# Kernel optimization log

Hardware: AMD Instinct MI355X
Metric: run time of the kernel (lower is better)

The kernel has to match this reference:

```python
import jax, jax.numpy as jnp
import numpy as np

H = 4          # attention_heads
TOPK = 101     # hard-coded [:101] in ContextModule.forward
EPS = 1e-5     # nn.LayerNorm default eps


def _linear(x, w, b):
    # torch nn.Linear: y = x @ W^T + b
    return x @ w.T + b


def _layer_norm(x, g, b):
    mu = jnp.mean(x, axis=-1, keepdims=True)
    var = jnp.var(x, axis=-1, keepdims=True)
    return (x - mu) * jax.lax.rsqrt(var + EPS) * g + b


def setup_inputs() -> dict:
    key = jax.random.key(0)
    ks = jax.random.split(key, 12)
    D, N, B, T = 512, 2000, 8, 1024
    s = 0.02
    f32 = jnp.float32
    return {
        "context_emb": jax.random.normal(ks[0], (N, D), f32),
        "encoder_out": jax.random.normal(ks[1], (B, T, D), f32),
        "wq": jax.random.normal(ks[2], (D, D), f32) * s,
        "bq": jnp.zeros((D,), f32),
        "wk": jax.random.normal(ks[3], (D, D), f32) * s,
        "bk": jnp.zeros((D,), f32),
        "wv": jax.random.normal(ks[4], (D, D), f32) * s,
        "bv": jnp.zeros((D,), f32),
        "wo": jax.random.normal(ks[5], (D, D), f32) * s,
        "bo": jnp.zeros((D,), f32),
        "w_comb": jax.random.normal(ks[6], (D, D), f32) * s,
        "b_comb": jnp.zeros((D,), f32),
        "ln_g": jnp.ones((D,), f32),
        "ln_b": jnp.zeros((D,), f32),
    }


def reference(context_emb, encoder_out, wq, bq, wk, bk, wv, bv, wo, bo,
              w_comb, b_comb, ln_g, ln_b):
    biasing_score = 1.0
    B, T, D = encoder_out.shape
    dk = D // H
    scale = 1.0 / np.sqrt(dk).astype(np.float32)

    # expand context to batch: [B, N, D]
    ctx = jnp.broadcast_to(context_emb, (B,) + context_emb.shape)

    # --- pass 1: attention matrix for scoring (get_attn_mat) ---
    q = _linear(encoder_out, wq, bq).reshape(B, T, H, dk).transpose(0, 2, 1, 3)  # bhtd
    k = _linear(ctx, wk, bk).reshape(B, -1, H, dk).transpose(0, 2, 1, 3)         # bhnd
    scores = jnp.einsum('bhtd,bhnd->bhtn', q, k) * scale
    attn = jax.nn.softmax(scores, axis=-1)                                        # [B,H,T,N]

    # attn_mat[0].sum(0).sum(0): per-context-phrase aggregate score -> [N]
    context_scores = attn[0].sum(axis=(0, 1))
    # torch.sort(descending)[1][:101] == top-101 indices by score
    _, idx = jax.lax.top_k(context_scores, TOPK)

    # gather filtered context embeddings: [B, 101, D]
    ctx_f = ctx[:, idx, :]

    # --- pass 2: full MHA on filtered context ---
    k2 = _linear(ctx_f, wk, bk).reshape(B, TOPK, H, dk).transpose(0, 2, 1, 3)
    v2 = _linear(ctx_f, wv, bv).reshape(B, TOPK, H, dk).transpose(0, 2, 1, 3)
    a2 = jax.nn.softmax(jnp.einsum('bhtd,bhnd->bhtn', q, k2) * scale, axis=-1)
    o = jnp.einsum('bhtn,bhnd->bhtd', a2, v2).transpose(0, 2, 1, 3).reshape(B, T, D)
    o = _linear(o, wo, bo)

    # combiner + residual + LayerNorm
    out = encoder_out + _linear(o, w_comb, b_comb) * biasing_score
    return _layer_norm(out, ln_g, ln_b)
```

## Files before the change

kernel.cpp:

```cpp
#include <hip/hip_runtime.h>
#include <hip/hip_bf16.h>


typedef short bhalf8 __attribute__((ext_vector_type(8)));
typedef float f32x4 __attribute__((ext_vector_type(4)));

#define SCALE 0.08838834764831845f

#define OFF_QBF    ((size_t)0)
#define OFF_RB     ((size_t)6193152)
#define OFF_TMP    ((size_t)8290304)
#define OFF_PART   (OFF_TMP)
#define OFF_CS     (OFF_TMP + 1024000)
#define OFF_IDX    (OFF_TMP + 1026048)
#define OFF_RSP    (OFF_TMP + 1026176)
#define OFF_CEBF   ((size_t)12484608)
#define OFF_K2BF   ((size_t)13022608)
#define OFF_V2TP   ((size_t)13074608)
#define OFF_WQBF   ((size_t)13107376)
#define OFF_WKBF   ((size_t)13238448)
#define OFF_WVBF   ((size_t)13369520)
#define OFF_WCBF   ((size_t)13500592)
#define OFF_WOTBF  ((size_t)13631664)
#define OFF_WC2BF  ((size_t)13762736)
#define OFF_BC2    ((size_t)13893808)

__device__ __forceinline__ float bf2f(short u) {
    union { float f; unsigned int i; } x;
    x.i = ((unsigned int)(unsigned short)u) << 16;
    return x.f;
}
__device__ __forceinline__ ushort f2b(float f) {
    union { float f; unsigned int i; } x; x.f = f;
    return (ushort)((x.i + 0x7fff + ((x.i >> 16) & 1)) >> 16);
}

__device__ __forceinline__ void gld16(ushort* lds, const ushort* g) {
    __builtin_amdgcn_global_load_lds(
        (const __attribute__((address_space(1))) unsigned int*)g,
        (__attribute__((address_space(3))) unsigned int*)lds, 16, 0, 0);
}

__global__ __launch_bounds__(256) void prep_kernel(
    const float* __restrict__ enc, const float* __restrict__ ce,
    const float* __restrict__ wq, const float* __restrict__ wk,
    const float* __restrict__ wv, const float* __restrict__ wc,
    const float* __restrict__ wo, const float* __restrict__ bo,
    const float* __restrict__ bcb,
    ushort* __restrict__ encbf, ushort* __restrict__ cebf,
    ushort* __restrict__ wqbf, ushort* __restrict__ wkbf,
    ushort* __restrict__ wvbf, ushort* __restrict__ wcbf,
    ushort* __restrict__ v2tp, ushort* __restrict__ wotbf,
    float* __restrict__ bc2)
{
    __shared__ float tile[32][33];
    const int b = blockIdx.x, tid = threadIdx.x;
    const float* s; ushort* d; int n4, base;
    if (b < 4096)      { s = enc; d = encbf; n4 = 1048576; base = b; }
    else if (b < 5096) { s = ce;  d = cebf;  n4 = 256000;  base = b - 4096; }
    else if (b < 5352) { s = wq;  d = wqbf;  n4 = 65536;   base = b - 5096; }
    else if (b < 5608) { s = wk;  d = wkbf;  n4 = 65536;   base = b - 5352; }
    else if (b < 5864) { s = wv;  d = wvbf;  n4 = 65536;   base = b - 5608; }
    else if (b < 6120) { s = wc;  d = wcbf;  n4 = 65536;   base = b - 5864; }
    else if (b < 6152) {
        const int i = (b - 6120) * 256 + tid;
        ((uint4*)v2tp)[i] = make_uint4(0u, 0u, 0u, 0u);
        return;
    } else if (b < 6154) {
        const int dd = (b - 6152) * 256 + tid;
        float acc = bcb[dd];
        const float4* wr = (const float4*)(wc + (size_t)dd * 512);
        const float4* br = (const float4*)bo;
        for (int m4 = 0; m4 < 128; ++m4) {
            const float4 w4 = wr[m4], b4 = br[m4];
            acc += w4.x * b4.x + w4.y * b4.y + w4.z * b4.z + w4.w * b4.w;
        }
        bc2[dd] = acc;
        return;
    } else {
        const int b2 = b - 6154;
        const int bx = (b2 & 15) * 32, by = (b2 >> 4) * 32;
        const int tx = tid & 31, ty = tid >> 5;
        #pragma unroll
        for (int rr = 0; rr < 4; ++rr)
            tile[ty + 8 * rr][tx] = wo[(size_t)(by + ty + 8 * rr) * 512 + bx + tx];
        __syncthreads();
        #pragma unroll
        for (int rr = 0; rr < 4; ++rr)
            wotbf[(size_t)(bx + ty + 8 * rr) * 512 + by + tx] =
                f2b(tile[tx][ty + 8 * rr]);
        return;
    }
    const int i = base * 256 + tid;
    if (i >= n4) return;
    const float4 v = ((const float4*)s)[i];
    ushort4 r;
    r.x = f2b(v.x); r.y = f2b(v.y); r.z = f2b(v.z); r.w = f2b(v.w);
    ((ushort4*)d)[i] = r;
}

__device__ __forceinline__ void stage_ab(
    const ushort* gA, const ushort* gB0, const ushort* gB1, int k0,
    ushort* As, ushort* Bs, int wave)
{
    gld16(As + wave * 512,        gA  + k0);
    gld16(As + 2048 + wave * 512, gA  + k0 + 32);
    gld16(Bs + wave * 512,        gB0 + k0);
    gld16(Bs + 4096 + wave * 512, gB0 + k0 + 32);
    gld16(Bs + 2048 + wave * 512, gB1 + k0);
    gld16(Bs + 6144 + wave * 512, gB1 + k0 + 32);
}

__device__ __forceinline__ void gemm_body_512(
    const ushort* A, const ushort* W, const float* bias, ushort* Cbf,
    int M, int bm, int bn, ushort* As, ushort* Bs, int rowA)
{
    const int tid = threadIdx.x;
    const int wave = tid >> 6, lane = tid & 63;
    const int wm = wave >> 1, wn = wave & 1;
    const int mr = lane & 15, g = lane >> 4;

    f32x4 acc[2][4];
    #pragma unroll
    for (int i = 0; i < 2; ++i)
        #pragma unroll
        for (int j = 0; j < 4; ++j)
            #pragma unroll
            for (int p = 0; p < 4; ++p) acc[i][j][p] = 0.f;

    const int r0 = tid >> 2, c0 = tid & 3;
    const int cA = (c0 ^ (r0 & 3)) * 8;
    const ushort* gA  = A + (size_t)rowA * 512 + cA;
    const ushort* gB0 = W + (size_t)(bn + r0) * 512 + cA;
    const ushort* gB1 = W + (size_t)(bn + r0 + 64) * 512 + cA;

    stage_ab(gA, gB0, gB1, 0, As, Bs, wave);
    for (int k0 = 0; k0 < 512; k0 += 64) {
        const int cur = (k0 >> 6) & 1;
        ushort* Ac = As + cur * 4096;
        ushort* Bc = Bs + cur * 8192;
        __syncthreads();
        if (k0 + 64 < 512)
            stage_ab(gA, gB0, gB1, k0 + 64,
                     As + (cur ^ 1) * 4096, Bs + (cur ^ 1) * 8192, wave);
        const int ksw = (g ^ (mr & 3)) << 3;
        #pragma unroll
        for (int h = 0; h < 2; ++h) {
            bhalf8 a[2], b[4];
            #pragma unroll
            for (int i = 0; i < 2; ++i)
                a[i] = *(const bhalf8*)
                    &Ac[h * 2048 + (wm * 32 + i * 16 + mr) * 32 + ksw];
            #pragma unroll
            for (int j = 0; j < 4; ++j)
                b[j] = *(const bhalf8*)
                    &Bc[h * 4096 + (wn * 64 + j * 16 + mr) * 32 + ksw];
            #pragma unroll
            for (int i = 0; i < 2; ++i)
                #pragma unroll
                for (int j = 0; j < 4; ++j)
                    acc[i][j] = __builtin_amdgcn_mfma_f32_16x16x32_bf16(
                        a[i], b[j], acc[i][j], 0, 0, 0);
        }
    }

    #pragma unroll
    for (int i = 0; i < 2; ++i) {
        #pragma unroll
        for (int j = 0; j < 4; ++j) {
            const int gn = bn + wn * 64 + j * 16 + mr;
            const float bb = bias ? bias[gn] : 0.f;
            #pragma unroll
            for (int p = 0; p < 4; ++p) {
                const int gm = bm + wm * 32 + i * 16 + g * 4 + p;
                if (gm >= M) continue;
                Cbf[(size_t)gm * 512 + gn] = f2b(acc[i][j][p] + bb);
            }
        }
    }
}

__global__ __launch_bounds__(256) void qkc_gemm(
    const ushort* __restrict__ encbf, const ushort* __restrict__ cebf,
    const ushort* __restrict__ wcbf,
    const ushort* __restrict__ wqbf, const ushort* __restrict__ wkbf,
    const ushort* __restrict__ wotbf,
    const float* __restrict__ bq, const float* __restrict__ bk,
    ushort* __restrict__ qbf, ushort* __restrict__ kcbf,
    ushort* __restrict__ wc2bf)
{
    __shared__ __align__(16) ushort As[2 * 64 * 64];
    __shared__ __align__(16) ushort Bs[2 * 128 * 64];
    const int z = blockIdx.z;
    if (z == 1 && blockIdx.y >= 32) return;
    if (z == 2 && blockIdx.y >= 8) return;
    const ushort* A = (z == 0) ? encbf : (z == 1) ? cebf : wcbf;
    const ushort* W = (z == 0) ? wqbf : (z == 1) ? wkbf : wotbf;
    const float* bias = (z == 0) ? bq : (z == 1) ? bk : nullptr;
    ushort* C = (z == 0) ? qbf : (z == 1) ? kcbf : wc2bf;
    const int M = (z == 0) ? 8192 : (z == 1) ? 2000 : 512;
    const int bm = blockIdx.y * 64;
    const int rowA = min(bm + (threadIdx.x >> 2), M - 1);
    gemm_body_512(A, W, bias, C, M, bm, blockIdx.x * 128, As, Bs, rowA);
}

__device__ __forceinline__ void stage_ktile(
    ushort* Ks, const ushort* kcbf, int nt, int h, int w, int lane)
{
    #pragma unroll
    for (int it = 0; it < 8; ++it) {
        const int u = it * 256 + (w << 6) + lane;
        const int nl = u >> 4, c = u & 15;
        gld16(Ks + (size_t)(it * 256 + (w << 6)) * 8,
              kcbf + (size_t)(nt * 128 + nl) * 512 + (h << 7)
                   + ((c ^ (nl & 7)) << 3));
    }
}

__device__ __forceinline__ void score_tile(
    const ushort* Ks, const bhalf8* aq, int mr, int g, f32x4* sacc)
{
    #pragma unroll
    for (int jn = 0; jn < 8; ++jn)
        #pragma unroll
        for (int p = 0; p < 4; ++p) sacc[jn][p] = 0.f;
    #pragma unroll
    for (int kd = 0; kd < 4; ++kd) {
        #pragma unroll
        for (int jn = 0; jn < 8; ++jn) {
            const int n = (jn << 4) + mr;
            const bhalf8 bk = *(const bhalf8*)
                &Ks[(n << 7) + ((((kd << 2) + g) ^ (n & 7)) << 3)];
            sacc[jn] = __builtin_amdgcn_mfma_f32_16x16x32_bf16(
                aq[kd], bk, sacc[jn], 0, 0, 0);
        }
    }
}

__global__ __launch_bounds__(256) void rowsum_part(
    const ushort* __restrict__ qb, const ushort* __restrict__ kcbf,
    float* __restrict__ rsp)
{
    __shared__ __align__(16) ushort Ks[2 * 128 * 128];
    const int tid = threadIdx.x, w = tid >> 6, lane = tid & 63;
    const int mr = lane & 15, g = lane >> 4;
    const int h = blockIdx.y, nc = blockIdx.z;
    const int bm = blockIdx.x * 64;

    const ushort* qrow = qb + (size_t)(bm + (w << 4) + mr) * 512 + (h << 7);
    bhalf8 aq[4];
    #pragma unroll
    for (int kd = 0; kd < 4; ++kd)
        aq[kd] = *(const bhalf8*)(qrow + (g << 3) + (kd << 5));

    const int nt0 = nc * 2, nt1 = nc * 2 + 1;
    stage_ktile(Ks, kcbf, nt0, h, w, lane);
    __syncthreads();
    stage_ktile(Ks + 16384, kcbf, nt1, h, w, lane);

    float rsl[4] = {0.f, 0.f, 0.f, 0.f};
    f32x4 sacc[8];
    score_tile(Ks, aq, mr, g, sacc);
    #pragma unroll
    for (int jn = 0; jn < 8; ++jn) {
        const bool valid = nt0 * 128 + (jn << 4) + mr < 2000;
        #pragma unroll
        for (int p = 0; p < 4; ++p)
            rsl[p] += valid ? __expf(sacc[jn][p] * SCALE) : 0.f;
    }
    __syncthreads();
    score_tile(Ks + 16384, aq, mr, g, sacc);
    #pragma unroll
    for (int jn = 0; jn < 8; ++jn) {
        const bool valid = nt1 * 128 + (jn << 4) + mr < 2000;
        #pragma unroll
        for (int p = 0; p < 4; ++p)
            rsl[p] += valid ? __expf(sacc[jn][p] * SCALE) : 0.f;
    }

    #pragma unroll
    for (int off = 1; off <= 8; off <<= 1)
        #pragma unroll
        for (int p = 0; p < 4; ++p)
            rsl[p] += __shfl_xor(rsl[p], off);
    if (mr == 0) {
        #pragma unroll
        for (int p = 0; p < 4; ++p) {
            const int row = (h << 10) + bm + (w << 4) + (g << 2) + p;
            rsp[(size_t)row * 8 + nc] = rsl[p];
        }
    }
}

__global__ __launch_bounds__(256) void colsum_part(
    const ushort* __restrict__ qb, const ushort* __restrict__ kcbf,
    const float* __restrict__ rsp, float* __restrict__ part)
{
    __shared__ __align__(16) ushort Ks[2 * 128 * 128];
    const int tid = threadIdx.x, w = tid >> 6, lane = tid & 63;
    const int mr = lane & 15, g = lane >> 4;
    const int h = blockIdx.y, nc = blockIdx.z;
    const int bm = blockIdx.x * 64;
    const int slot = ((h * 16 + blockIdx.x) << 2) + w;

    const ushort* qrow = qb + (size_t)(bm + (w << 4) + mr) * 512 + (h << 7);
    bhalf8 aq[4];
    #pragma unroll
    for (int kd = 0; kd < 4; ++kd)
        aq[kd] = *(const bhalf8*)(qrow + (g << 3) + (kd << 5));

    float inv[4];
    #pragma unroll
    for (int p = 0; p < 4; ++p) {
        const int row = (h << 10) + bm + (w << 4) + (g << 2) + p;
        const float4 ra = *(const float4*)(rsp + (size_t)row * 8);
        const float4 rb = *(const float4*)(rsp + (size_t)row * 8 + 4);
        inv[p] = 1.f / (ra.x + ra.y + ra.z + ra.w + rb.x + rb.y + rb.z + rb.w);
    }

    const int nt0 = nc * 2, nt1 = nc * 2 + 1;
    stage_ktile(Ks, kcbf, nt0, h, w, lane);
    __syncthreads();
    stage_ktile(Ks + 16384, kcbf, nt1, h, w, lane);

    f32x4 sacc[8];
    #pragma unroll
    for (int t = 0; t < 2; ++t) {
        if (t == 1) __syncthreads();
        const int nt = t ? nt1 : nt0;
        score_tile(t ? Ks + 16384 : Ks, aq, mr, g, sacc);
        #pragma unroll
        for (int jn = 0; jn < 8; ++jn) {
            const int n = nt * 128 + (jn << 4) + mr;
            const bool valid = n < 2000;
            float cv = 0.f;
            #pragma unroll
            for (int p = 0; p < 4; ++p)
                cv += valid ? __expf(sacc[jn][p] * SCALE) * inv[p] : 0.f;
            cv += __shfl_xor(cv, 16);
            cv += __shfl_xor(cv, 32);
            if (g == 0 && valid) part[(size_t)slot * 2000 + n] = cv;
        }
    }
}

__global__ __launch_bounds__(256) void reduce_full_kernel(
    const float* __restrict__ part, float* __restrict__ cs)
{
    const int n = blockIdx.x * 256 + threadIdx.x;
    if (n >= 2000) return;
    float s = 0.f;
    for (int sl = 0; sl < 256; ++sl) s += part[(size_t)sl * 2000 + n];
    cs[n] = s;
}

__global__ void topk_kernel(const float* __restrict__ cs,
                            int* __restrict__ idx)
{
    const int lane = threadIdx.x;
    const unsigned long long below = (1ull << lane) - 1ull;

    unsigned key[32];
    #pragma unroll
    for (int i = 0; i < 32; ++i) {
        const int n = lane + 64 * i;
        const float s = (n < 2000) ? cs[n] : -1e30f;
        const unsigned u = __float_as_uint(s);
        key[i] = u ^ ((unsigned)((int)u >> 31) | 0x80000000u);
    }

    unsigned prefix = 0;
    int remaining = 101;
    for (int b = 31; b >= 0; --b) {
        const unsigned tgt = (prefix << 1) | 1u;
        int cnt = 0;
        #pragma unroll
        for (int i = 0; i < 32; ++i)
            cnt += (int)__popcll(__ballot((key[i] >> b) == tgt));
        if (cnt >= remaining) prefix = tgt;
        else { remaining -= cnt; prefix = prefix << 1; }
    }
    const unsigned T = prefix;

    int base = 0;
    #pragma unroll
    for (int i = 0; i < 32; ++i) {
        const unsigned long long m = __ballot(key[i] > T);
        if (key[i] > T) idx[base + (int)__popcll(m & below)] = lane + 64 * i;
        base += (int)__popcll(m);
    }
    int r = remaining;
    #pragma unroll
    for (int i = 0; i < 32; ++i) {
        const unsigned long long m = __ballot(key[i] == T);
        const int cb = (int)__popcll(m & below);
        if (key[i] == T && cb < r) idx[base + cb] = lane + 64 * i;
        const int take = min(r, (int)__popcll(m));
        base += take; r -= take;
    }
}

__global__ __launch_bounds__(256) void kv2_proj(
    const ushort* __restrict__ cebf, const int* __restrict__ idxbuf,
    const ushort* __restrict__ wkbf, const ushort* __restrict__ wvbf,
    const float* __restrict__ bk, const float* __restrict__ bv,
    ushort* __restrict__ k2bf, ushort* __restrict__ v2tp)
{
    __shared__ __align__(16) ushort As[2 * 64 * 64];
    __shared__ __align__(16) ushort Bs[2 * 128 * 64];
    const int z = blockIdx.z;
    const ushort* W = z ? wvbf : wkbf;
    const float* bias = z ? bv : bk;
    const int tid = threadIdx.x;
    const int wave = tid >> 6, lane = tid & 63;
    const int wm = wave >> 1, wn = wave & 1;
    const int mr = lane & 15, g = lane >> 4;
    const int bm = blockIdx.y * 64, bn = blockIdx.x * 128;

    f32x4 acc[2][4];
    #pragma unroll
    for (int i = 0; i < 2; ++i)
        #pragma unroll
        for (int j = 0; j < 4; ++j)
            #pragma unroll
            for (int p = 0; p < 4; ++p) acc[i][j][p] = 0.f;

    const int r0 = tid >> 2, c0 = tid & 3;
    const int cA = (c0 ^ (r0 & 3)) * 8;
    const int rA  = min(bm + r0, 100);
    const int srcrow = idxbuf[rA];
    const ushort* gA  = cebf + (size_t)srcrow * 512 + cA;
    const ushort* gB0 = W + (size_t)(bn + r0) * 512 + cA;
    const ushort* gB1 = W + (size_t)(bn + r0 + 64) * 512 + cA;

    stage_ab(gA, gB0, gB1, 0, As, Bs, wave);
    for (int k0 = 0; k0 < 512; k0 += 64) {
        const int cur = (k0 >> 6) & 1;
        ushort* Ac = As + cur * 4096;
        ushort* Bc = Bs + cur * 8192;
        __syncthreads();
        if (k0 + 64 < 512)
            stage_ab(gA, gB0, gB1, k0 + 64,
                     As + (cur ^ 1) * 4096, Bs + (cur ^ 1) * 8192, wave);
        const int ksw = (g ^ (mr & 3)) << 3;
        #pragma unroll
        for (int h = 0; h < 2; ++h) {
            bhalf8 a[2], b[4];
            #pragma unroll
            for (int i = 0; i < 2; ++i)
                a[i] = *(const bhalf8*)
                    &Ac[h * 2048 + (wm * 32 + i * 16 + mr) * 32 + ksw];
            #pragma unroll
            for (int j = 0; j < 4; ++j)
                b[j] = *(const bhalf8*)
                    &Bc[h * 4096 + (wn * 64 + j * 16 + mr) * 32 + ksw];
            #pragma unroll
            for (int i = 0; i < 2; ++i)
                #pragma unroll
                for (int j = 0; j < 4; ++j)
                    acc[i][j] = __builtin_amdgcn_mfma_f32_16x16x32_bf16(
                        a[i], b[j], acc[i][j], 0, 0, 0);
        }
    }

    #pragma unroll
    for (int i = 0; i < 2; ++i) {
        #pragma unroll
        for (int j = 0; j < 4; ++j) {
            const int gn = bn + wn * 64 + j * 16 + mr;
            const float bb = bias[gn];
            #pragma unroll
            for (int p = 0; p < 4; ++p) {
                const int gm = bm + wm * 32 + i * 16 + g * 4 + p;
                if (gm >= 101) continue;
                const ushort v = f2b(acc[i][j][p] + bb);
                if (z == 0) k2bf[(size_t)gm * 512 + gn] = v;
                else        v2tp[(size_t)gn * 128 + gm] = v;
            }
        }
    }
}

__global__ __launch_bounds__(512) void attn2_fused(
    const ushort* __restrict__ qb, const ushort* __restrict__ k2bf,
    const ushort* __restrict__ v2tp, ushort* __restrict__ obf)
{
    __shared__ __align__(16) ushort K2s[128 * 128];
    __shared__ __align__(16) ushort V2s[128 * 128];
    __shared__ __align__(16) ushort Ps[8 * 16 * 128];
    const int tid = threadIdx.x, w = tid >> 6, lane = tid & 63;
    const int mr = lane & 15, g = lane >> 4;
    const int h = blockIdx.y;
    const int bm = blockIdx.x * 128;

    #pragma unroll
    for (int it = 0; it < 4; ++it) {
        const int cl = tid + 512 * it;
        const int n = cl >> 4, c = cl & 15;
        uint4 kv = make_uint4(0u, 0u, 0u, 0u);
        if (n < 101)
            kv = *(const uint4*)(k2bf + (size_t)n * 512 + h * 128 + c * 8);
        *(uint4*)&K2s[(n << 7) + ((c ^ (n & 7)) << 3)] = kv;
        const uint4 vv = *(const uint4*)(v2tp + (((size_t)h << 7) + n) * 128 + c * 8);
        *(uint4*)&V2s[(n << 7) + ((c ^ (n & 7)) << 3)] = vv;
    }
    __syncthreads();

    f32x4 sacc[8];
    #pragma unroll
    for (int jn = 0; jn < 8; ++jn)
        #pragma unroll
        for (int p = 0; p < 4; ++p) sacc[jn][p] = 0.f;
    const ushort* qrow = qb + (size_t)(bm + (w << 4) + mr) * 512 + (h << 7);
    #pragma unroll
    for (int kd = 0; kd < 4; ++kd) {
        const bhalf8 aq = *(const bhalf8*)(qrow + (g << 3) + (kd << 5));
        #pragma unroll
        for (int jn = 0; jn < 8; ++jn) {
            const int n = (jn << 4) + mr;
            const bhalf8 bk = *(const bhalf8*)
                &K2s[(n << 7) + ((((kd << 2) + g) ^ (n & 7)) << 3)];
            sacc[jn] = __builtin_amdgcn_mfma_f32_16x16x32_bf16(aq, bk, sacc[jn], 0, 0, 0);
        }
    }

    float mrow[4] = {-1e30f, -1e30f, -1e30f, -1e30f};
    #pragma unroll
    for (int jn = 0; jn < 8; ++jn) {
        const bool valid = (jn < 6) || (jn == 6 && mr < 5);
        #pragma unroll
        for (int p = 0; p < 4; ++p) {
            const float s = valid ? sacc[jn][p] * SCALE : -1e30f;
            sacc[jn][p] = s;
            mrow[p] = fmaxf(mrow[p], s);
        }
    }
    #pragma unroll
    for (int off = 1; off <= 8; off <<= 1)
        #pragma unroll
        for (int p = 0; p < 4; ++p)
            mrow[p] = fmaxf(mrow[p], __shfl_xor(mrow[p], off));
    float srow[4] = {0.f, 0.f, 0.f, 0.f};
    #pragma unroll
    for (int jn = 0; jn < 8; ++jn)
        #pragma unroll
        for (int p = 0; p < 4; ++p) {
            const float e = __expf(sacc[jn][p] - mrow[p]);
            sacc[jn][p] = e;
            srow[p] += e;
        }
    #pragma unroll
    for (int off = 1; off <= 8; off <<= 1)
        #pragma unroll
        for (int p = 0; p < 4; ++p)
            srow[p] += __shfl_xor(srow[p], off);
    float inv[4];
    #pragma unroll
    for (int p = 0; p < 4; ++p) inv[p] = 1.f / srow[p];

    ushort* pw = Ps + (w << 11);
    #pragma unroll
    for (int jn = 0; jn < 8; ++jn) {
        const int cb = (jn << 1) + (mr >> 3);
        #pragma unroll
        for (int p = 0; p < 4; ++p) {
            const int r = (g << 2) + p;
            pw[(r << 7) + ((cb ^ (r & 7)) << 3) + (mr & 7)] =
                f2b(sacc[jn][p] * inv[p]);
        }
    }

    f32x4 oacc[8];
    #pragma unroll
    for (int jd = 0; jd < 8; ++jd)
        #pragma unroll
        for (int p = 0; p < 4; ++p) oacc[jd][p] = 0.f;
    #pragma unroll
    for (int kn = 0; kn < 4; ++kn) {
        const int ck = (kn << 2) + g;
        const bhalf8 ap = *(const bhalf8*)
            &pw[(mr << 7) + ((ck ^ (mr & 7)) << 3)];
        #pragma unroll
        for (int jd = 0; jd < 8; ++jd) {
            const int d = (jd << 4) + mr;
            const bhalf8 bv = *(const bhalf8*)
                &V2s[(d << 7) + ((ck ^ (d & 7)) << 3)];
            oacc[jd] = __builtin_amdgcn_mfma_f32_16x16x32_bf16(ap, bv, oacc[jd], 0, 0, 0);
        }
    }

    #pragma unroll
    for (int jd = 0; jd < 8; ++jd)
        #pragma unroll
        for (int p = 0; p < 4; ++p) {
            const int row = bm + (w << 4) + (g << 2) + p;
            obf[(size_t)row * 512 + (h << 7) + (jd << 4) + mr] = f2b(oacc[jd][p]);
        }
}

__device__ __forceinline__ void pl_stage(
    const ushort* gA, const ushort* gB, int k0,
    ushort* Asb, ushort* Bsb, int w)
{
    if (w < 2) {
        gld16(Asb + w * 512,        gA + k0);
        gld16(Asb + 1024 + w * 512, gA + k0 + 32);
    }
    #pragma unroll
    for (int r = 0; r < 8; ++r) {
        const int nb = r * 4 + w;
        gld16(Bsb + nb * 512,         gB + nb * 8192 + k0);
        gld16(Bsb + 16384 + nb * 512, gB + nb * 8192 + k0 + 32);
    }
}

__global__ __launch_bounds__(256) void proj_ln(
    const ushort* __restrict__ obf, const ushort* __restrict__ wc2bf,
    const float* __restrict__ bc2, const float* __restrict__ enc,
    const float* __restrict__ gw, const float* __restrict__ bta,
    float* __restrict__ out)
{
    __shared__ __align__(16) ushort As[2 * 2048];
    __shared__ __align__(16) ushort Bs[2 * 32768];
    __shared__ float red1[2][32], red2[2][32];
    const int tid = threadIdx.x, w = tid >> 6, lane = tid & 63;
    const int mr = lane & 15, gq = lane >> 4;
    const int rh = w & 1, ch = w >> 1;
    const int bm = blockIdx.x * 32;

    f32x4 acc[16];
    #pragma unroll
    for (int j = 0; j < 16; ++j)
        #pragma unroll
        for (int p = 0; p < 4; ++p) acc[j][p] = 0.f;

    const int lr = lane >> 2, lc = lane & 3;
    const int swc = (lc ^ (lr & 3)) * 8;
    const ushort* gA = obf + (size_t)(bm + ((w & 1) << 4) + lr) * 512 + swc;
    const ushort* gB = wc2bf + (size_t)lr * 512 + swc;

    pl_stage(gA, gB, 0, As, Bs, w);
    for (int k0 = 0; k0 < 512; k0 += 64) {
        const int cur = (k0 >> 6) & 1;
        ushort* Ac = As + cur * 2048;
        ushort* Bc = Bs + cur * 32768;
        __syncthreads();
        if (k0 + 64 < 512)
            pl_stage(gA, gB, k0 + 64,
                     As + (cur ^ 1) * 2048, Bs + (cur ^ 1) * 32768, w);
        const int ksw = (gq ^ (mr & 3)) << 3;
        #pragma unroll
        for (int h = 0; h < 2; ++h) {
            const bhalf8 a = *(const bhalf8*)
                &Ac[h * 1024 + (((rh << 4) + mr) << 5) + ksw];
            #pragma unroll
            for (int j = 0; j < 16; ++j) {
                const int n = (ch << 8) + (j << 4) + mr;
                const bhalf8 b = *(const bhalf8*)
                    &Bc[h * 16384 + (n << 5) + ksw];
                acc[j] = __builtin_amdgcn_mfma_f32_16x16x32_bf16(a, b, acc[j], 0, 0, 0);
            }
        }
    }

    float s1[4] = {0.f, 0.f, 0.f, 0.f}, s2[4] = {0.f, 0.f, 0.f, 0.f};
    #pragma unroll
    for (int j = 0; j < 16; ++j) {
        const int gcol = (ch << 8) + (j << 4) + mr;
        const float bb = bc2[gcol];
        #pragma unroll
        for (int p = 0; p < 4; ++p) {
            const int grow = bm + (rh << 4) + (gq << 2) + p;
            const float x = acc[j][p] + bb + enc[(size_t)grow * 512 + gcol];
            acc[j][p] = x;
            s1[p] += x;
            s2[p] += x * x;
        }
    }
    #pragma unroll
    for (int off = 1; off <= 8; off <<= 1)
        #pragma unroll
        for (int p = 0; p < 4; ++p) {
            s1[p] += __shfl_xor(s1[p], off);
            s2[p] += __shfl_xor(s2[p], off);
        }
    if (mr == 0) {
        #pragma unroll
        for (int p = 0; p < 4; ++p) {
            red1[ch][(rh << 4) + (gq << 2) + p] = s1[p];
            red2[ch][(rh << 4) + (gq << 2) + p] = s2[p];
        }
    }
    __syncthreads();
    float mu[4], rstd[4];
    #pragma unroll
    for (int p = 0; p < 4; ++p) {
        const int ri = (rh << 4) + (gq << 2) + p;
        const float t1 = red1[0][ri] + red1[1][ri];
        const float t2 = red2[0][ri] + red2[1][ri];
        const float m = t1 * (1.f / 512.f);
        mu[p] = m;
        rstd[p] = rsqrtf(t2 * (1.f / 512.f) - m * m + 1e-5f);
    }
    #pragma unroll
    for (int j = 0; j < 16; ++j) {
        const int gcol = (ch << 8) + (j << 4) + mr;
        const float gg = gw[gcol], bb = bta[gcol];
        #pragma unroll
        for (int p = 0; p < 4; ++p) {
            const int grow = bm + (rh << 4) + (gq << 2) + p;
            out[(size_t)grow * 512 + gcol] = (acc[j][p] - mu[p]) * rstd[p] * gg + bb;
        }
    }
}

extern "C" void kernel_launch(void* const* d_in, const int* in_sizes, int n_in,
                              void* d_out, int out_size, void* d_ws, size_t ws_size,
                              hipStream_t stream)
{
    const float* ce  = (const float*)d_in[0];
    const float* enc = (const float*)d_in[1];
    const float* wq  = (const float*)d_in[2];
    const float* bq  = (const float*)d_in[3];
    const float* wk  = (const float*)d_in[4];
    const float* bk  = (const float*)d_in[5];
    const float* wv  = (const float*)d_in[6];
    const float* bv  = (const float*)d_in[7];
    const float* wo  = (const float*)d_in[8];
    const float* bo  = (const float*)d_in[9];
    const float* wc  = (const float*)d_in[10];
    const float* bcb = (const float*)d_in[11];
    const float* lng = (const float*)d_in[12];
    const float* lnb = (const float*)d_in[13];
    float* ws  = (float*)d_ws;
    float* out = (float*)d_out;

    ushort* qbf    = (ushort*)(ws + OFF_QBF);
    ushort* encbf  = (ushort*)(ws + OFF_RB);
    ushort* kcbf   = (ushort*)(ws + OFF_RB);
    ushort* obf    = (ushort*)(ws + OFF_RB);
    float*  part   = ws + OFF_PART;
    float*  cs     = ws + OFF_CS;
    int*    idx    = (int*)(ws + OFF_IDX);
    float*  rsp    = ws + OFF_RSP;
    ushort* cebf   = (ushort*)(ws + OFF_CEBF);
    ushort* k2bf   = (ushort*)(ws + OFF_K2BF);
    ushort* v2tp   = (ushort*)(ws + OFF_V2TP);
    ushort* wqbf   = (ushort*)(ws + OFF_WQBF);
    ushort* wkbf   = (ushort*)(ws + OFF_WKBF);
    ushort* wvbf   = (ushort*)(ws + OFF_WVBF);
    ushort* wcbf   = (ushort*)(ws + OFF_WCBF);
    ushort* wotbf  = (ushort*)(ws + OFF_WOTBF);
    ushort* wc2bf  = (ushort*)(ws + OFF_WC2BF);
    float*  bc2    = ws + OFF_BC2;

    prep_kernel<<<6410, 256, 0, stream>>>(enc, ce, wq, wk, wv, wc, wo, bo, bcb,
                                          encbf, cebf, wqbf, wkbf, wvbf, wcbf,
                                          v2tp, wotbf, bc2);
    qkc_gemm<<<dim3(4, 128, 3), 256, 0, stream>>>(encbf, cebf, wcbf,
                                                  wqbf, wkbf, wotbf,
                                                  bq, bk, qbf, kcbf, wc2bf);
    rowsum_part<<<dim3(16, 4, 8), 256, 0, stream>>>(qbf, kcbf, rsp);
    colsum_part<<<dim3(16, 4, 8), 256, 0, stream>>>(qbf, kcbf, rsp, part);
    reduce_full_kernel<<<8, 256, 0, stream>>>(part, cs);
    topk_kernel<<<1, 64, 0, stream>>>(cs, idx);
    kv2_proj<<<dim3(4, 2, 2), 256, 0, stream>>>(cebf, idx, wkbf, wvbf, bk, bv,
                                                k2bf, v2tp);
    attn2_fused<<<dim3(64, 4), 512, 0, stream>>>(qbf, k2bf, v2tp, obf);
    proj_ln<<<256, 256, 0, stream>>>(obf, wc2bf, bc2, enc, lng, lnb, out);
    (void)in_sizes; (void)n_in; (void)out_size; (void)ws_size;
}
```

Measured before the change: 136.0 us.

## Fuse rowsum and colsum passes into one cooperative kernel with grid sync

Merges the rowsum and colsum kernels into a single cooperative launch that computes the scores once, keeps the exponentials in registers, and uses a grid-wide sync before the column sums. This removes the second K-tile staging, the repeated MFMA score computation and exp, and one kernel launch. The qkc_gemm grid is also flattened to 672 blocks so no early-exit blocks are launched. In exchange it holds more live registers for the two exp tiles and relies on all 512 blocks being co-resident for the grid sync.

```diff
diff --git a/kernel.cpp b/kernel.cpp
--- a/kernel.cpp
+++ b/kernel.cpp
@@ -1,5 +1,8 @@
 #include <hip/hip_runtime.h>
 #include <hip/hip_bf16.h>
+#include <hip/hip_cooperative_groups.h>
+
+namespace cg = cooperative_groups;
 
 
 typedef short bhalf8 __attribute__((ext_vector_type(8)));
@@ -191,17 +194,19 @@
 {
     __shared__ __align__(16) ushort As[2 * 64 * 64];
     __shared__ __align__(16) ushort Bs[2 * 128 * 64];
-    const int z = blockIdx.z;
-    if (z == 1 && blockIdx.y >= 32) return;
-    if (z == 2 && blockIdx.y >= 8) return;
+    const int bid = blockIdx.x;
+    int z, x, y;
+    if (bid < 512)      { z = 0; x = bid & 3; y = bid >> 2; }
+    else if (bid < 640) { z = 1; x = (bid - 512) & 3; y = (bid - 512) >> 2; }
+    else                { z = 2; x = (bid - 640) & 3; y = (bid - 640) >> 2; }
     const ushort* A = (z == 0) ? encbf : (z == 1) ? cebf : wcbf;
     const ushort* W = (z == 0) ? wqbf : (z == 1) ? wkbf : wotbf;
     const float* bias = (z == 0) ? bq : (z == 1) ? bk : nullptr;
     ushort* C = (z == 0) ? qbf : (z == 1) ? kcbf : wc2bf;
     const int M = (z == 0) ? 8192 : (z == 1) ? 2000 : 512;
-    const int bm = blockIdx.y * 64;
+    const int bm = y * 64;
     const int rowA = min(bm + (threadIdx.x >> 2), M - 1);
-    gemm_body_512(A, W, bias, C, M, bm, blockIdx.x * 128, As, Bs, rowA);
+    gemm_body_512(A, W, bias, C, M, bm, x * 128, As, Bs, rowA);
 }
 
 __device__ __forceinline__ void stage_ktile(
@@ -237,64 +242,9 @@
     }
 }
 
-__global__ __launch_bounds__(256) void rowsum_part(
+__global__ __launch_bounds__(256) void stage1_fused(
     const ushort* __restrict__ qb, const ushort* __restrict__ kcbf,
-    float* __restrict__ rsp)
-{
-    __shared__ __align__(16) ushort Ks[2 * 128 * 128];
-    const int tid = threadIdx.x, w = tid >> 6, lane = tid & 63;
-    const int mr = lane & 15, g = lane >> 4;
-    const int h = blockIdx.y, nc = blockIdx.z;
-    const int bm = blockIdx.x * 64;
-
-    const ushort* qrow = qb + (size_t)(bm + (w << 4) + mr) * 512 + (h << 7);
-    bhalf8 aq[4];
-    #pragma unroll
-    for (int kd = 0; kd < 4; ++kd)
-        aq[kd] = *(const bhalf8*)(qrow + (g << 3) + (kd << 5));
-
-    const int nt0 = nc * 2, nt1 = nc * 2 + 1;
-    stage_ktile(Ks, kcbf, nt0, h, w, lane);
-    __syncthreads();
-    stage_ktile(Ks + 16384, kcbf, nt1, h, w, lane);
-
-    float rsl[4] = {0.f, 0.f, 0.f, 0.f};
-    f32x4 sacc[8];
-    score_tile(Ks, aq, mr, g, sacc);
-    #pragma unroll
-    for (int jn = 0; jn < 8; ++jn) {
-        const bool valid = nt0 * 128 + (jn << 4) + mr < 2000;
-        #pragma unroll
-        for (int p = 0; p < 4; ++p)
-            rsl[p] += valid ? __expf(sacc[jn][p] * SCALE) : 0.f;
-    }
-    __syncthreads();
-    score_tile(Ks + 16384, aq, mr, g, sacc);
-    #pragma unroll
-    for (int jn = 0; jn < 8; ++jn) {
-        const bool valid = nt1 * 128 + (jn << 4) + mr < 2000;
-        #pragma unroll
-        for (int p = 0; p < 4; ++p)
-            rsl[p] += valid ? __expf(sacc[jn][p] * SCALE) : 0.f;
-    }
-
-    #pragma unroll
-    for (int off = 1; off <= 8; off <<= 1)
-        #pragma unroll
-        for (int p = 0; p < 4; ++p)
-            rsl[p] += __shfl_xor(rsl[p], off);
-    if (mr == 0) {
-        #pragma unroll
-        for (int p = 0; p < 4; ++p) {
-            const int row = (h << 10) + bm + (w << 4) + (g << 2) + p;
-            rsp[(size_t)row * 8 + nc] = rsl[p];
-        }
-    }
-}
-
-__global__ __launch_bounds__(256) void colsum_part(
-    const ushort* __restrict__ qb, const ushort* __restrict__ kcbf,
-    const float* __restrict__ rsp, float* __restrict__ part)
+    float* __restrict__ rsp, float* __restrict__ part)
 {
     __shared__ __align__(16) ushort Ks[2 * 128 * 128];
     const int tid = threadIdx.x, w = tid >> 6, lane = tid & 63;
@@ -309,6 +259,52 @@
     for (int kd = 0; kd < 4; ++kd)
         aq[kd] = *(const bhalf8*)(qrow + (g << 3) + (kd << 5));
 
+    const int nt0 = nc * 2, nt1 = nc * 2 + 1;
+    stage_ktile(Ks, kcbf, nt0, h, w, lane);
+    __syncthreads();
+    stage_ktile(Ks + 16384, kcbf, nt1, h, w, lane);
+
+    float rsl[4] = {0.f, 0.f, 0.f, 0.f};
+    f32x4 e0[8], e1[8];
+    score_tile(Ks, aq, mr, g, e0);
+    #pragma unroll
+    for (int jn = 0; jn < 8; ++jn) {
+        const bool valid = nt0 * 128 + (jn << 4) + mr < 2000;
+        #pragma unroll
+        for (int p = 0; p < 4; ++p) {
+            const float ev = valid ? __expf(e0[jn][p] * SCALE) : 0.f;
+            e0[jn][p] = ev;
+            rsl[p] += ev;
+        }
+    }
+    __syncthreads();
+    score_tile(Ks + 16384, aq, mr, g, e1);
+    #pragma unroll
+    for (int jn = 0; jn < 8; ++jn) {
+        const bool valid = nt1 * 128 + (jn << 4) + mr < 2000;
+        #pragma unroll
+        for (int p = 0; p < 4; ++p) {
+            const float ev = valid ? __expf(e1[jn][p] * SCALE) : 0.f;
+            e1[jn][p] = ev;
+            rsl[p] += ev;
+        }
+    }
+
+    #pragma unroll
+    for (int off = 1; off <= 8; off <<= 1)
+        #pragma unroll
+        for (int p = 0; p < 4; ++p)
+            rsl[p] += __shfl_xor(rsl[p], off);
+    if (mr == 0) {
+        #pragma unroll
+        for (int p = 0; p < 4; ++p) {
+            const int row = (h << 10) + bm + (w << 4) + (g << 2) + p;
+            rsp[(size_t)row * 8 + nc] = rsl[p];
+        }
+    }
+
+    cg::this_grid().sync();
+
     float inv[4];
     #pragma unroll
     for (int p = 0; p < 4; ++p) {
@@ -318,17 +314,9 @@
         inv[p] = 1.f / (ra.x + ra.y + ra.z + ra.w + rb.x + rb.y + rb.z + rb.w);
     }
 
-    const int nt0 = nc * 2, nt1 = nc * 2 + 1;
-    stage_ktile(Ks, kcbf, nt0, h, w, lane);
-    __syncthreads();
-    stage_ktile(Ks + 16384, kcbf, nt1, h, w, lane);
-
-    f32x4 sacc[8];
     #pragma unroll
     for (int t = 0; t < 2; ++t) {
-        if (t == 1) __syncthreads();
         const int nt = t ? nt1 : nt0;
-        score_tile(t ? Ks + 16384 : Ks, aq, mr, g, sacc);
         #pragma unroll
         for (int jn = 0; jn < 8; ++jn) {
             const int n = nt * 128 + (jn << 4) + mr;
@@ -336,7 +324,7 @@
             float cv = 0.f;
             #pragma unroll
             for (int p = 0; p < 4; ++p)
-                cv += valid ? __expf(sacc[jn][p] * SCALE) * inv[p] : 0.f;
+                cv += (t ? e1[jn][p] : e0[jn][p]) * inv[p];
             cv += __shfl_xor(cv, 16);
             cv += __shfl_xor(cv, 32);
             if (g == 0 && valid) part[(size_t)slot * 2000 + n] = cv;
@@ -757,11 +745,15 @@
     prep_kernel<<<6410, 256, 0, stream>>>(enc, ce, wq, wk, wv, wc, wo, bo, bcb,
                                           encbf, cebf, wqbf, wkbf, wvbf, wcbf,
                                           v2tp, wotbf, bc2);
-    qkc_gemm<<<dim3(4, 128, 3), 256, 0, stream>>>(encbf, cebf, wcbf,
-                                                  wqbf, wkbf, wotbf,
-                                                  bq, bk, qbf, kcbf, wc2bf);
-    rowsum_part<<<dim3(16, 4, 8), 256, 0, stream>>>(qbf, kcbf, rsp);
-    colsum_part<<<dim3(16, 4, 8), 256, 0, stream>>>(qbf, kcbf, rsp, part);
+    qkc_gemm<<<672, 256, 0, stream>>>(encbf, cebf, wcbf, wqbf, wkbf, wotbf,
+                                      bq, bk, qbf, kcbf, wc2bf);
+    {
+        const ushort* a0 = qbf; const ushort* a1 = kcbf;
+        float* a2 = rsp; float* a3 = part;
+        void* args[] = {(void*)&a0, (void*)&a1, (void*)&a2, (void*)&a3};
+        hipLaunchCooperativeKernel((void*)stage1_fused, dim3(16, 4, 8),
+                                   dim3(256), args, 0, stream);
+    }
     reduce_full_kernel<<<8, 256, 0, stream>>>(part, cs);
     topk_kernel<<<1, 64, 0, stream>>>(cs, idx);
     kv2_proj<<<dim3(4, 2, 2), 256, 0, stream>>>(cebf, idx, wkbf, wvbf, bk, bv,
```

After: 210.3 us. 54.6% more time.
